# Kernel optimization log

Hardware: AMD Instinct MI355X
Metric: run time of the kernel (lower is better)

## Reference

```python
import jax, jax.numpy as jnp
import numpy as np

B, FEAT = 2048, 256
NUM_PIDS, CQ_SIZE = 30000, 8192
MOMENTUM = 0.5
SCALAR = 30.0
EPS_BN = 1e-5      # BatchNorm1d default eps
EPS_NORM = 1e-12   # F.normalize default eps


def l2norm(x):
    n = jnp.linalg.norm(x, axis=1, keepdims=True)
    return x / jnp.maximum(n, EPS_NORM)


def setup_inputs() -> dict:
    key = jax.random.key(0)
    k1, k2, k3, k4 = jax.random.split(key, 4)
    inputs = jax.random.normal(k1, (B, FEAT), jnp.float32)
    label = jax.random.randint(k2, (B,), 0, NUM_PIDS + 1)  # NUM_PIDS == ignore_index
    lut = jax.random.normal(k3, (NUM_PIDS, FEAT), jnp.float32)
    cq = jax.random.normal(k4, (CQ_SIZE, FEAT), jnp.float32)
    bn_weight = jnp.ones((FEAT,), jnp.float32)
    bn_bias = jnp.zeros((FEAT,), jnp.float32)
    return {"inputs": inputs, "label": label, "lut": lut, "cq": cq,
            "bn_weight": bn_weight, "bn_bias": bn_bias}


def reference(inputs, label, lut, cq, bn_weight, bn_bias):
    dtype = inputs.dtype
    rows = jnp.arange(B)

    # --- eval-mode BN on inputs (running stats at init: mean=0, var=1) ---
    norm_inputs = inputs / jnp.sqrt(jnp.asarray(1.0 + EPS_BN, dtype)) * bn_weight + bn_bias

    # --- bad-row masks (rows that are all zero) ---
    bad_lut_mask = jnp.all(lut == 0, axis=1)            # [P]
    good_lut = ~bad_lut_mask
    lc = jnp.minimum(label, NUM_PIDS - 1)
    bad_pos_mask = (label < NUM_PIDS) & bad_lut_mask[lc]  # label hits a bad lut row

    # --- train-mode masked BN over good lut rows (momentum=1.0 => running stats = batch stats) ---
    gm = good_lut[:, None].astype(dtype)
    n = jnp.sum(gm)
    mean = jnp.sum(lut * gm, axis=0) / n
    var = jnp.sum(((lut - mean) ** 2) * gm, axis=0) / n  # biased var for normalization
    lut_bn = jnp.where(good_lut[:, None],
                       (lut - mean) / jnp.sqrt(var + EPS_BN) * bn_weight + bn_bias,
                       lut)
    # running stats update happens under the hood (detached); unbiased var
    rm1 = jax.lax.stop_gradient(mean)
    rv1 = jax.lax.stop_gradient(var * n / (n - 1.0))

    qn = l2norm(norm_inputs)                              # [B, F]
    out_lab = qn @ l2norm(lut_bn).T                       # [B, P]
    out_lab = jnp.where(bad_lut_mask[None, :], jnp.asarray(-1.0, dtype), out_lab)
    out_lab = out_lab.at[rows, lc].set(
        jnp.where(bad_pos_mask, jnp.asarray(1.0, dtype), out_lab[rows, lc]))

    # --- eval-mode masked BN on cq using the just-updated running stats ---
    bad_cq_mask = jnp.all(cq == 0, axis=1)                # [Q]
    cq_bn = jnp.where(~bad_cq_mask[:, None],
                      (cq - rm1) / jnp.sqrt(rv1 + EPS_BN) * bn_weight + bn_bias,
                      cq)
    out_unl = qn @ l2norm(cq_bn).T                        # [B, Q]
    out_unl = jnp.where(bad_cq_mask[None, :], jnp.asarray(-1.0, dtype), out_unl)

    projected = jnp.concatenate([out_lab, out_unl], axis=1) * jnp.asarray(SCALAR, dtype)

    # --- cross entropy with ignore_index = NUM_PIDS, reduction='none', then sum/B ---
    logp = jax.nn.log_softmax(projected, axis=1)
    valid = label != NUM_PIDS
    per = -logp[rows, jnp.where(valid, label, 0)]
    per = jnp.where(valid, per, jnp.asarray(0.0, dtype))
    loss = jnp.sum(per) / B

    # --- serial momentum scatter into lut + circular-buffer enqueue into cq ---
    xs = jax.lax.stop_gradient(inputs)
    lut0 = jax.lax.stop_gradient(lut)
    cq0 = jax.lax.stop_gradient(cq)

    def step(carry, xy):
        lut_c, cq_c, hdr = carry
        x, y = xy
        is_lab = y < NUM_PIDS
        yc = jnp.minimum(y, NUM_PIDS - 1)
        new_row = jnp.where(is_lab, MOMENTUM * lut_c[yc] + (1.0 - MOMENTUM) * x, lut_c[yc])
        lut_c = lut_c.at[yc].set(new_row)
        cq_row = jnp.where(is_lab, cq_c[hdr], x)
        cq_c = cq_c.at[hdr].set(cq_row)
        hdr = jnp.where(is_lab, hdr, (hdr + 1) % CQ_SIZE)
        return (lut_c, cq_c, hdr), None

    (new_lut, new_cq, _), _ = jax.lax.scan(
        step, (lut0, cq0, jnp.asarray(0, label.dtype)), (xs, label))

    return loss, new_lut, new_cq
```

## Files before the change

### kernel.cpp

```cpp
#include <hip/hip_runtime.h>
#include <math.h>

#define NUM_PIDS 30000
#define CQ_SIZE  8192
#define BATCH    2048
#define FEAT     256
#define EPS_BN   1e-5f
#define EPS_NORM 1e-12f
#define SCALARV  30.0f

#define LUT_PAD  30080
#define NCOL     38272
#define BC       128
#define LUT_TILES 235
#define CT       299
#define RT       16
#define NWG      (CT*RT)
#define NB1      240
#define ROWS1    125
#define QPLANE   (BATCH*FEAT)

#define WS_Q1    0
#define WS_CB1   (WS_Q1 + BATCH*FEAT)
#define WS_CB2   (WS_CB1 + BATCH)
#define WS_RN2   (WS_CB2 + BATCH)
#define WS_FLAGS (WS_RN2 + 2*NCOL)
#define WS_PSUM  (WS_FLAGS + LUT_PAD)
#define WS_PSQ   (WS_PSUM + NB1*FEAT)
#define WS_PCNT  (WS_PSQ + NB1*FEAT)
#define WS_A1    (WS_PCNT + 256)
#define WS_B1    (WS_A1 + FEAT)
#define WS_A2    (WS_B1 + FEAT)
#define WS_B2    (WS_A2 + FEAT)
#define WS_ZT    (WS_B2 + FEAT)
#define WS_PART  (WS_ZT + BATCH)
#define WS_LOSS8 (WS_PART + BATCH*CT)
#define WS_XH    ((WS_LOSS8 + 8 + 3) & ~3)
#define WS_XL    (WS_XH + NCOL*FEAT/2)
#define WS_QP    (WS_XL + NCOL*FEAT/2)

typedef __bf16 bf16x8 __attribute__((ext_vector_type(8)));
typedef float  f32x4  __attribute__((ext_vector_type(4)));

__device__ __forceinline__ unsigned short f2bf(float f) {
  __bf16 h = (__bf16)f; return __builtin_bit_cast(unsigned short, h);
}
__device__ __forceinline__ float bf2f(unsigned short u) {
  __bf16 h = __builtin_bit_cast(__bf16, u); return (float)h;
}
__device__ __forceinline__ void gload_lds16(const void* g, void* l) {
  __builtin_amdgcn_global_load_lds((__attribute__((address_space(1))) void*)(g),
                                   (__attribute__((address_space(3))) void*)(l), 16, 0, 0);
}
__device__ __forceinline__ void stage8(const unsigned short* g, unsigned char* d) {
#pragma unroll
  for (int i = 0; i < 8; ++i)
    gload_lds16(g + (size_t)i * 16 * FEAT, d + i * 1024);
}

__global__ __launch_bounds__(256) void k_stats1(const float* __restrict__ lut,
                                                float* __restrict__ ws,
                                                int* __restrict__ flags) {
  const int t = threadIdx.x;
  const int rbase = blockIdx.x * ROWS1;
  __shared__ unsigned char wz[ROWS1 * 4];
  float s = 0.f, sq = 0.f;
  for (int i = 0; i < ROWS1; ++i) {
    float v = lut[(size_t)(rbase + i) * FEAT + t];
    s += v; sq += v * v;
    unsigned long long bal = __ballot(v != 0.0f);
    if ((t & 63) == 0) wz[i * 4 + (t >> 6)] = (bal != 0ull) ? 1 : 0;
  }
  __syncthreads();
  for (int i = t; i < ROWS1; i += 256) {
    int bad = !(wz[i*4] | wz[i*4+1] | wz[i*4+2] | wz[i*4+3]);
    flags[rbase + i] = bad;
  }
  ws[WS_PSUM + blockIdx.x * FEAT + t] = s;
  ws[WS_PSQ  + blockIdx.x * FEAT + t] = sq;
  if (t == 0) {
    int cnt = 0;
    for (int i = 0; i < ROWS1; ++i)
      cnt += (wz[i*4] | wz[i*4+1] | wz[i*4+2] | wz[i*4+3]) ? 1 : 0;
    ws[WS_PCNT + blockIdx.x] = (float)cnt;
  }
}

__global__ __launch_bounds__(256) void k_stats2(const float* __restrict__ bnw,
                                                const float* __restrict__ bnb,
                                                float* __restrict__ ws) {
  const int t = threadIdx.x;
  float2* rn2 = (float2*)(ws + WS_RN2);
  float s = 0.f, sq = 0.f, n = 0.f;
  for (int b = 0; b < NB1; ++b) { s += ws[WS_PSUM + b*FEAT + t]; sq += ws[WS_PSQ + b*FEAT + t]; }
  for (int b = 0; b < NB1; ++b) n += ws[WS_PCNT + b];
  float mean = s / n;
  float var = fmaxf(sq / n - mean * mean, 0.f);
  float istd_b = rsqrtf(var + EPS_BN);
  float rv1 = var * n / (n - 1.f);
  float istd_u = rsqrtf(rv1 + EPS_BN);
  float w = bnw[t], b_ = bnb[t];
  float a1 = istd_b * w, a2 = istd_u * w;
  ws[WS_A1 + t] = a1; ws[WS_B1 + t] = b_ - mean * a1;
  ws[WS_A2 + t] = a2; ws[WS_B2 + t] = b_ - mean * a2;
  if (t < (LUT_PAD - NUM_PIDS)) rn2[NUM_PIDS + t] = make_float2(0.f, -1e30f);
}

__global__ __launch_bounds__(256) void k_split(const float* __restrict__ lut,
                                               const float* __restrict__ cq,
                                               unsigned short* __restrict__ xh,
                                               unsigned short* __restrict__ xl) {
  const int stride = gridDim.x * blockDim.x;
  for (int u = blockIdx.x * blockDim.x + threadIdx.x; u < NCOL * 32; u += stride) {
    int col = u >> 5, k8 = (u & 31) * 8;
    float v[8];
    if (col < NUM_PIDS) {
      const float4* p = (const float4*)&lut[(size_t)col * FEAT + k8];
      float4 a = p[0], b = p[1];
      v[0]=a.x; v[1]=a.y; v[2]=a.z; v[3]=a.w; v[4]=b.x; v[5]=b.y; v[6]=b.z; v[7]=b.w;
    } else if (col < LUT_PAD) {
#pragma unroll
      for (int j = 0; j < 8; ++j) v[j] = 0.f;
    } else {
      const float4* p = (const float4*)&cq[(size_t)(col - LUT_PAD) * FEAT + k8];
      float4 a = p[0], b = p[1];
      v[0]=a.x; v[1]=a.y; v[2]=a.z; v[3]=a.w; v[4]=b.x; v[5]=b.y; v[6]=b.z; v[7]=b.w;
    }
    unsigned int hp[4], lp[4];
#pragma unroll
    for (int j = 0; j < 4; ++j) {
      unsigned short h0 = f2bf(v[2*j]),   h1 = f2bf(v[2*j+1]);
      unsigned short l0 = f2bf(v[2*j]   - bf2f(h0));
      unsigned short l1 = f2bf(v[2*j+1] - bf2f(h1));
      hp[j] = (unsigned int)h0 | ((unsigned int)h1 << 16);
      lp[j] = (unsigned int)l0 | ((unsigned int)l1 << 16);
    }
    size_t off = (size_t)col * FEAT + k8;
    *(uint4*)(xh + off) = make_uint4(hp[0], hp[1], hp[2], hp[3]);
    *(uint4*)(xl + off) = make_uint4(lp[0], lp[1], lp[2], lp[3]);
  }
}

__global__ __launch_bounds__(256) void k_qn(const float* __restrict__ inp,
                                            const float* __restrict__ bnw,
                                            const float* __restrict__ bnb,
                                            float* __restrict__ ws,
                                            unsigned short* __restrict__ qp) {
  const int r = blockIdx.x, t = threadIdx.x;
  const float s0 = rsqrtf(1.0f + EPS_BN);
  float v = inp[(size_t)r * FEAT + t];
  float bn = v * (bnw[t] * s0) + bnb[t];
  float x = bn * bn;
  for (int o = 32; o; o >>= 1) x += __shfl_down(x, o);
  __shared__ float w4[4];
  __shared__ float w8[8];
  if ((t & 63) == 0) w4[t >> 6] = x;
  __syncthreads();
  float nsq = w4[0] + w4[1] + w4[2] + w4[3];
  float rinv = 1.0f / fmaxf(sqrtf(nsq), EPS_NORM);
  float qn = bn * rinv;
  float y1 = qn * ws[WS_B1 + t], y2 = qn * ws[WS_B2 + t];
  for (int o = 32; o; o >>= 1) { y1 += __shfl_down(y1, o); y2 += __shfl_down(y2, o); }
  if ((t & 63) == 0) { w8[t >> 6] = y1; w8[4 + (t >> 6)] = y2; }
  float q1 = qn * ws[WS_A1 + t], q2 = qn * ws[WS_A2 + t];
  ws[WS_Q1 + (size_t)r * FEAT + t] = q1;
  size_t o1 = (size_t)r * FEAT + t;
  unsigned short h1 = f2bf(q1), h2 = f2bf(q2);
  qp[0*QPLANE + o1] = h1;
  qp[1*QPLANE + o1] = f2bf(q1 - bf2f(h1));
  qp[2*QPLANE + o1] = h2;
  qp[3*QPLANE + o1] = f2bf(q2 - bf2f(h2));
  __syncthreads();
  if (t == 0) {
    ws[WS_CB1 + r] = w8[0] + w8[1] + w8[2] + w8[3];
    ws[WS_CB2 + r] = w8[4] + w8[5] + w8[6] + w8[7];
  }
}

__global__ __launch_bounds__(256) void k_norms(const float* __restrict__ lut,
                                               const float* __restrict__ cq,
                                               float* __restrict__ ws) {
  const int row = blockIdx.x * 4 + (threadIdx.x >> 6);
  const int ln = threadIdx.x & 63;
  if (row >= NUM_PIDS + CQ_SIZE) return;
  float2* rn2 = (float2*)(ws + WS_RN2);
  const float* src; const float* av; const float* bv; int cidx;
  if (row < NUM_PIDS) {
    src = lut + (size_t)row * FEAT; av = ws + WS_A1; bv = ws + WS_B1; cidx = row;
  } else {
    int q = row - NUM_PIDS;
    src = cq + (size_t)q * FEAT; av = ws + WS_A2; bv = ws + WS_B2; cidx = LUT_PAD + q;
  }
  float4 x = ((const float4*)src)[ln];
  float4 a = ((const float4*)av)[ln];
  float4 b = ((const float4*)bv)[ln];
  bool nz = (x.x != 0.f) || (x.y != 0.f) || (x.z != 0.f) || (x.w != 0.f);
  unsigned long long bal = __ballot(nz);
  float t0 = a.x*x.x + b.x, t1 = a.y*x.y + b.y, t2 = a.z*x.z + b.z, t3 = a.w*x.w + b.w;
  float ssum = t0*t0 + t1*t1 + t2*t2 + t3*t3;
  for (int o = 32; o; o >>= 1) ssum += __shfl_xor(ssum, o);
  if (ln == 0) {
    rn2[cidx] = (bal == 0ull) ? make_float2(0.f, -SCALARV)
                              : make_float2(1.0f / fmaxf(sqrtf(ssum), EPS_NORM), 1e30f);
  }
}

__global__ __launch_bounds__(256) void k_gemm(const unsigned short* __restrict__ xh,
                                              const unsigned short* __restrict__ xl,
                                              const unsigned short* __restrict__ qp,
                                              float* __restrict__ ws) {
  __shared__ __align__(16) unsigned char smem[65536];
  const int tid = threadIdx.x;
  const int w = tid >> 6, l = tid & 63;
  const int bid = blockIdx.x;
  const int sid = (bid & 7) * (NWG / 8) + (bid >> 3);
  const int colT = sid >> 4, rowT = sid & 15;
  const bool islut = colT < LUT_TILES;
  const int colbase = colT * BC;
  const int rowbase = rowT * 128;

  const unsigned short* qh = qp + (islut ? 0 : 2) * QPLANE;
  const unsigned short* ql = qh + QPLANE;

  const unsigned short* gsrc;
  unsigned char* lbase;
  int gbase;
  if (w == 0)      { gsrc = xh; lbase = smem;         gbase = colbase; }
  else if (w == 1) { gsrc = xl; lbase = smem + 16384; gbase = colbase; }
  else if (w == 2) { gsrc = qh; lbase = smem + 32768; gbase = rowbase; }
  else             { gsrc = ql; lbase = smem + 49152; gbase = rowbase; }

  const int kchunk = (l & 3) ^ ((l >> 4) & 3);
  const unsigned short* gp = gsrc + (size_t)(gbase + (l >> 2)) * FEAT + kchunk * 8;

  const int lc = l & 15, lk = l >> 4;
  const int wr = w >> 1, wc = w & 1;
  const int roff = (lk ^ ((lc >> 2) & 3)) * 16;

  f32x4 acc[4][4];
#pragma unroll
  for (int rf = 0; rf < 4; ++rf)
#pragma unroll
    for (int cf = 0; cf < 4; ++cf) { f32x4 z = {0.f,0.f,0.f,0.f}; acc[rf][cf] = z; }

  stage8(gp, lbase);
  for (int s = 0; s < 8; ++s) {
    const int cur = s & 1;
    if (s < 7) {
      stage8(gp + (s + 1) * 32, lbase + (cur ^ 1) * 8192);
      asm volatile("s_waitcnt vmcnt(8)" ::: "memory");
    } else {
      asm volatile("s_waitcnt vmcnt(0)" ::: "memory");
    }
    __builtin_amdgcn_s_barrier();
    __builtin_amdgcn_sched_barrier(0);
    bf16x8 ah[4], al[4], bh[4], bl[4];
#pragma unroll
    for (int rf = 0; rf < 4; ++rf) {
      int off = cur * 8192 + (wr * 64 + rf * 16 + lc) * 64 + roff;
      ah[rf] = *(const bf16x8*)(smem + 32768 + off);
      al[rf] = *(const bf16x8*)(smem + 49152 + off);
    }
#pragma unroll
    for (int cf = 0; cf < 4; ++cf) {
      int off = cur * 8192 + (wc * 64 + cf * 16 + lc) * 64 + roff;
      bh[cf] = *(const bf16x8*)(smem + off);
      bl[cf] = *(const bf16x8*)(smem + 16384 + off);
    }
#pragma unroll
    for (int rf = 0; rf < 4; ++rf)
#pragma unroll
      for (int cf = 0; cf < 4; ++cf) {
        acc[rf][cf] = __builtin_amdgcn_mfma_f32_16x16x32_bf16(ah[rf], bh[cf], acc[rf][cf], 0, 0, 0);
        acc[rf][cf] = __builtin_amdgcn_mfma_f32_16x16x32_bf16(ah[rf], bl[cf], acc[rf][cf], 0, 0, 0);
        acc[rf][cf] = __builtin_amdgcn_mfma_f32_16x16x32_bf16(al[rf], bh[cf], acc[rf][cf], 0, 0, 0);
      }
    if (s < 7) __builtin_amdgcn_s_barrier();
  }

  const float* cb = ws + (islut ? WS_CB1 : WS_CB2);
  const float2* rn2 = (const float2*)(ws + WS_RN2);
  float* red = (float*)smem;
#pragma unroll
  for (int rf = 0; rf < 4; ++rf) {
    float cbv[4];
#pragma unroll
    for (int r4 = 0; r4 < 4; ++r4)
      cbv[r4] = cb[rowbase + wr * 64 + rf * 16 + lk * 4 + r4];
    float part[4] = {0.f, 0.f, 0.f, 0.f};
#pragma unroll
    for (int cf = 0; cf < 4; ++cf) {
      float2 rc = rn2[colbase + wc * 64 + cf * 16 + lc];
#pragma unroll
      for (int r4 = 0; r4 < 4; ++r4) {
        float z = SCALARV * rc.x * (acc[rf][cf][r4] + cbv[r4]);
        z = fminf(z, rc.y);
        part[r4] += __expf(z - SCALARV);
      }
    }
#pragma unroll
    for (int r4 = 0; r4 < 4; ++r4) {
#pragma unroll
      for (int o = 1; o < 16; o <<= 1) part[r4] += __shfl_xor(part[r4], o);
      if (lc == 0) red[(wr * 64 + rf * 16 + lk * 4 + r4) * 2 + wc] = part[r4];
    }
  }
  __syncthreads();
  if (tid < 128) {
    float val = red[tid * 2] + red[tid * 2 + 1];
    ws[WS_PART + (size_t)colT * BATCH + rowbase + tid] = val;
  }
}

__global__ __launch_bounds__(256) void k_target(const int* __restrict__ label,
                                                const float* __restrict__ lut,
                                                float* __restrict__ ws) {
  const int r = blockIdx.x, t = threadIdx.x;
  const int* flags = (const int*)(ws + WS_FLAGS);
  const float2* rn2 = (const float2*)(ws + WS_RN2);
  int y = label[r];
  if (y >= NUM_PIDS) { if (t == 0) ws[WS_ZT + r] = 0.f; return; }
  if (flags[y] == 1) { if (t == 0) ws[WS_ZT + r] = SCALARV; return; }
  float x = ws[WS_Q1 + (size_t)r * FEAT + t] * lut[(size_t)y * FEAT + t];
  for (int o = 32; o; o >>= 1) x += __shfl_down(x, o);
  __shared__ float w4[4];
  if ((t & 63) == 0) w4[t >> 6] = x;
  __syncthreads();
  if (t == 0) {
    float dot = w4[0] + w4[1] + w4[2] + w4[3];
    ws[WS_ZT + r] = SCALARV * rn2[y].x * (dot + ws[WS_CB1 + r]);
  }
}

__global__ __launch_bounds__(256) void k_loss(const int* __restrict__ label,
                                              float* __restrict__ ws) {
  const int t = threadIdx.x;
  const int r = blockIdx.x * 256 + t;
  const int* flags = (const int*)(ws + WS_FLAGS);
  float ls = 0.f;
  int y = label[r];
  if (y < NUM_PIDS) {
    float ss = 0.f;
    const float* p = ws + WS_PART;
    for (int c = 0; c < CT; ++c) ss += p[(size_t)c * BATCH + r];
    if (flags[y] == 1) ss += 1.0f - __expf(-2.0f * SCALARV);
    ls = (SCALARV + __logf(ss)) - ws[WS_ZT + r];
  }
  for (int o = 32; o; o >>= 1) ls += __shfl_down(ls, o);
  __shared__ float w4[4];
  if ((t & 63) == 0) w4[t >> 6] = ls;
  __syncthreads();
  if (t == 0) ws[WS_LOSS8 + blockIdx.x] = w4[0] + w4[1] + w4[2] + w4[3];
}

__global__ void k_loss2(float* __restrict__ ws, float* __restrict__ out) {
  if (threadIdx.x == 0) {
    float s = 0.f;
    for (int i = 0; i < 8; ++i) s += ws[WS_LOSS8 + i];
    out[0] = s / (float)BATCH;
  }
}

__global__ __launch_bounds__(256) void k_lutupd(const int* __restrict__ label,
                                                const float* __restrict__ inp,
                                                const float* __restrict__ lut,
                                                float* __restrict__ out_lut) {
  const int r = blockIdx.x, t = threadIdx.x;
  const int y = label[r];
  if (y >= NUM_PIDS) return;
  __shared__ unsigned long long mask[32];
  const int wv = t >> 6, ln = t & 63;
#pragma unroll
  for (int it = 0; it < 8; ++it) {
    int i = it * 256 + wv * 64 + ln;
    unsigned long long bal = __ballot(label[i] == y);
    if (ln == 0) mask[it * 4 + wv] = bal;
  }
  __syncthreads();
  const int wr_ = r >> 6, br_ = r & 63;
  unsigned long long selfbit = 1ull << br_;
  bool after = (mask[wr_] & ~((selfbit - 1) | selfbit)) != 0ull;
  for (int w2 = wr_ + 1; w2 < 32; ++w2) after = after || (mask[w2] != 0ull);
  if (after) return;
  float f = lut[(size_t)y * FEAT + t];
  for (int w2 = 0; w2 <= wr_; ++w2) {
    unsigned long long m = mask[w2];
    if (w2 == wr_) m &= (selfbit - 1) | selfbit;
    while (m) {
      int b = __ffsll((unsigned long long)m) - 1;
      m &= m - 1;
      int rr = w2 * 64 + b;
      f = 0.5f * f + 0.5f * inp[(size_t)rr * FEAT + t];
    }
  }
  out_lut[(size_t)y * FEAT + t] = f;
}

__global__ __launch_bounds__(256) void k_cqupd(const int* __restrict__ label,
                                               const float* __restrict__ inp,
                                               float* __restrict__ out_cq) {
  const int r = blockIdx.x, t = threadIdx.x;
  if (label[r] != NUM_PIDS) return;
  __shared__ unsigned long long mask[32];
  const int wv = t >> 6, ln = t & 63;
#pragma unroll
  for (int it = 0; it < 8; ++it) {
    int i = it * 256 + wv * 64 + ln;
    unsigned long long bal = __ballot(label[i] == NUM_PIDS);
    if (ln == 0) mask[it * 4 + wv] = bal;
  }
  __syncthreads();
  const int wr_ = r >> 6, br_ = r & 63;
  int rank = 0;
  for (int w2 = 0; w2 < wr_; ++w2) rank += __popcll(mask[w2]);
  rank += __popcll(mask[wr_] & ((1ull << br_) - 1ull));
  out_cq[(size_t)rank * FEAT + t] = inp[(size_t)r * FEAT + t];
}

extern "C" void kernel_launch(void* const* d_in, const int* in_sizes, int n_in,
                              void* d_out, int out_size, void* d_ws, size_t ws_size,
                              hipStream_t stream) {
  const float* inp = (const float*)d_in[0];
  const int* label = (const int*)d_in[1];
  const float* lut = (const float*)d_in[2];
  const float* cq  = (const float*)d_in[3];
  const float* bnw = (const float*)d_in[4];
  const float* bnb = (const float*)d_in[5];
  float* out = (float*)d_out;
  float* ws  = (float*)d_ws;
  int* flags = (int*)(ws + WS_FLAGS);
  unsigned short* xh = (unsigned short*)(ws + WS_XH);
  unsigned short* xl = (unsigned short*)(ws + WS_XL);
  unsigned short* qp = (unsigned short*)(ws + WS_QP);

  float* out_lut = out + 1;
  float* out_cq  = out + 1 + (size_t)NUM_PIDS * FEAT;

  hipMemcpyAsync(out_lut, lut, (size_t)NUM_PIDS * FEAT * sizeof(float),
                 hipMemcpyDeviceToDevice, stream);
  hipMemcpyAsync(out_cq, cq, (size_t)CQ_SIZE * FEAT * sizeof(float),
                 hipMemcpyDeviceToDevice, stream);

  k_split<<<2048, 256, 0, stream>>>(lut, cq, xh, xl);
  k_stats1<<<NB1, 256, 0, stream>>>(lut, ws, flags);
  k_stats2<<<1, 256, 0, stream>>>(bnw, bnb, ws);
  k_qn<<<BATCH, 256, 0, stream>>>(inp, bnw, bnb, ws, qp);
  k_norms<<<(NUM_PIDS + CQ_SIZE + 3) / 4, 256, 0, stream>>>(lut, cq, ws);
  k_gemm<<<NWG, 256, 0, stream>>>(xh, xl, qp, ws);
  k_target<<<BATCH, 256, 0, stream>>>(label, lut, ws);
  k_loss<<<8, 256, 0, stream>>>(label, ws);
  k_loss2<<<1, 64, 0, stream>>>(ws, out);
  k_lutupd<<<BATCH, 256, 0, stream>>>(label, inp, lut, out_lut);
  k_cqupd<<<BATCH, 256, 0, stream>>>(label, inp, out_cq);
}
```

Measured before the change: 374.0 us.

## Fuse split and norm kernels; restructure GEMM to stage only B tiles in LDS

Merges the bf16 hi/lo split kernel and the row-norm kernel into one per-row prep kernel, so lut and cq are read once instead of twice and a launch is dropped. The GEMM now stages only the lut/cq hi/lo tiles in LDS, loading 64-wide K chunks with an XOR swizzle. The query operand is read directly from global memory into registers. LDS use is halved and launch bounds request 3 blocks per CU for more occupancy, but the double-buffered prefetch is gone, so loads and MFMA no longer overlap, and direct global query loads may add latency.

```diff
diff --git a/kernel.cpp b/kernel.cpp
--- a/kernel.cpp
+++ b/kernel.cpp
@@ -52,11 +52,6 @@
   __builtin_amdgcn_global_load_lds((__attribute__((address_space(1))) void*)(g),
                                    (__attribute__((address_space(3))) void*)(l), 16, 0, 0);
 }
-__device__ __forceinline__ void stage8(const unsigned short* g, unsigned char* d) {
-#pragma unroll
-  for (int i = 0; i < 8; ++i)
-    gload_lds16(g + (size_t)i * 16 * FEAT, d + i * 1024);
-}
 
 __global__ __launch_bounds__(256) void k_stats1(const float* __restrict__ lut,
                                                 float* __restrict__ ws,
@@ -106,38 +101,44 @@
   if (t < (LUT_PAD - NUM_PIDS)) rn2[NUM_PIDS + t] = make_float2(0.f, -1e30f);
 }
 
-__global__ __launch_bounds__(256) void k_split(const float* __restrict__ lut,
-                                               const float* __restrict__ cq,
-                                               unsigned short* __restrict__ xh,
-                                               unsigned short* __restrict__ xl) {
-  const int stride = gridDim.x * blockDim.x;
-  for (int u = blockIdx.x * blockDim.x + threadIdx.x; u < NCOL * 32; u += stride) {
-    int col = u >> 5, k8 = (u & 31) * 8;
-    float v[8];
-    if (col < NUM_PIDS) {
-      const float4* p = (const float4*)&lut[(size_t)col * FEAT + k8];
-      float4 a = p[0], b = p[1];
-      v[0]=a.x; v[1]=a.y; v[2]=a.z; v[3]=a.w; v[4]=b.x; v[5]=b.y; v[6]=b.z; v[7]=b.w;
-    } else if (col < LUT_PAD) {
-#pragma unroll
-      for (int j = 0; j < 8; ++j) v[j] = 0.f;
-    } else {
-      const float4* p = (const float4*)&cq[(size_t)(col - LUT_PAD) * FEAT + k8];
-      float4 a = p[0], b = p[1];
-      v[0]=a.x; v[1]=a.y; v[2]=a.z; v[3]=a.w; v[4]=b.x; v[5]=b.y; v[6]=b.z; v[7]=b.w;
-    }
-    unsigned int hp[4], lp[4];
-#pragma unroll
-    for (int j = 0; j < 4; ++j) {
-      unsigned short h0 = f2bf(v[2*j]),   h1 = f2bf(v[2*j+1]);
-      unsigned short l0 = f2bf(v[2*j]   - bf2f(h0));
-      unsigned short l1 = f2bf(v[2*j+1] - bf2f(h1));
-      hp[j] = (unsigned int)h0 | ((unsigned int)h1 << 16);
-      lp[j] = (unsigned int)l0 | ((unsigned int)l1 << 16);
-    }
-    size_t off = (size_t)col * FEAT + k8;
-    *(uint4*)(xh + off) = make_uint4(hp[0], hp[1], hp[2], hp[3]);
-    *(uint4*)(xl + off) = make_uint4(lp[0], lp[1], lp[2], lp[3]);
+__global__ __launch_bounds__(256) void k_prep(const float* __restrict__ lut,
+                                              const float* __restrict__ cq,
+                                              float* __restrict__ ws,
+                                              unsigned short* __restrict__ xh,
+                                              unsigned short* __restrict__ xl) {
+  const int row = blockIdx.x * 4 + (threadIdx.x >> 6);
+  const int ln = threadIdx.x & 63;
+  float2* rn2 = (float2*)(ws + WS_RN2);
+  if (row >= NUM_PIDS && row < LUT_PAD) {
+    uint2 z = make_uint2(0u, 0u);
+    *(uint2*)(xh + (size_t)row * FEAT + ln * 4) = z;
+    *(uint2*)(xl + (size_t)row * FEAT + ln * 4) = z;
+    return;
+  }
+  const float* src; const float* av; const float* bv;
+  if (row < NUM_PIDS) {
+    src = lut + (size_t)row * FEAT; av = ws + WS_A1; bv = ws + WS_B1;
+  } else {
+    src = cq + (size_t)(row - LUT_PAD) * FEAT; av = ws + WS_A2; bv = ws + WS_B2;
+  }
+  float4 x = ((const float4*)src)[ln];
+  float4 a = ((const float4*)av)[ln];
+  float4 b = ((const float4*)bv)[ln];
+  unsigned short h0 = f2bf(x.x), h1 = f2bf(x.y), h2 = f2bf(x.z), h3 = f2bf(x.w);
+  unsigned short l0 = f2bf(x.x - bf2f(h0)), l1 = f2bf(x.y - bf2f(h1));
+  unsigned short l2 = f2bf(x.z - bf2f(h2)), l3 = f2bf(x.w - bf2f(h3));
+  *(uint2*)(xh + (size_t)row * FEAT + ln * 4) =
+      make_uint2((unsigned)h0 | ((unsigned)h1 << 16), (unsigned)h2 | ((unsigned)h3 << 16));
+  *(uint2*)(xl + (size_t)row * FEAT + ln * 4) =
+      make_uint2((unsigned)l0 | ((unsigned)l1 << 16), (unsigned)l2 | ((unsigned)l3 << 16));
+  bool nz = (x.x != 0.f) || (x.y != 0.f) || (x.z != 0.f) || (x.w != 0.f);
+  unsigned long long bal = __ballot(nz);
+  float t0 = a.x*x.x + b.x, t1 = a.y*x.y + b.y, t2 = a.z*x.z + b.z, t3 = a.w*x.w + b.w;
+  float ssum = t0*t0 + t1*t1 + t2*t2 + t3*t3;
+  for (int o = 32; o; o >>= 1) ssum += __shfl_xor(ssum, o);
+  if (ln == 0) {
+    rn2[row] = (bal == 0ull) ? make_float2(0.f, -SCALARV)
+                             : make_float2(1.0f / fmaxf(sqrtf(ssum), EPS_NORM), 1e30f);
   }
 }
 
@@ -177,39 +178,11 @@
   }
 }
 
-__global__ __launch_bounds__(256) void k_norms(const float* __restrict__ lut,
-                                               const float* __restrict__ cq,
-                                               float* __restrict__ ws) {
-  const int row = blockIdx.x * 4 + (threadIdx.x >> 6);
-  const int ln = threadIdx.x & 63;
-  if (row >= NUM_PIDS + CQ_SIZE) return;
-  float2* rn2 = (float2*)(ws + WS_RN2);
-  const float* src; const float* av; const float* bv; int cidx;
-  if (row < NUM_PIDS) {
-    src = lut + (size_t)row * FEAT; av = ws + WS_A1; bv = ws + WS_B1; cidx = row;
-  } else {
-    int q = row - NUM_PIDS;
-    src = cq + (size_t)q * FEAT; av = ws + WS_A2; bv = ws + WS_B2; cidx = LUT_PAD + q;
-  }
-  float4 x = ((const float4*)src)[ln];
-  float4 a = ((const float4*)av)[ln];
-  float4 b = ((const float4*)bv)[ln];
-  bool nz = (x.x != 0.f) || (x.y != 0.f) || (x.z != 0.f) || (x.w != 0.f);
-  unsigned long long bal = __ballot(nz);
-  float t0 = a.x*x.x + b.x, t1 = a.y*x.y + b.y, t2 = a.z*x.z + b.z, t3 = a.w*x.w + b.w;
-  float ssum = t0*t0 + t1*t1 + t2*t2 + t3*t3;
-  for (int o = 32; o; o >>= 1) ssum += __shfl_xor(ssum, o);
-  if (ln == 0) {
-    rn2[cidx] = (bal == 0ull) ? make_float2(0.f, -SCALARV)
-                              : make_float2(1.0f / fmaxf(sqrtf(ssum), EPS_NORM), 1e30f);
-  }
-}
-
-__global__ __launch_bounds__(256) void k_gemm(const unsigned short* __restrict__ xh,
-                                              const unsigned short* __restrict__ xl,
-                                              const unsigned short* __restrict__ qp,
-                                              float* __restrict__ ws) {
-  __shared__ __align__(16) unsigned char smem[65536];
+__global__ __launch_bounds__(256, 3) void k_gemm(const unsigned short* __restrict__ xh,
+                                                 const unsigned short* __restrict__ xl,
+                                                 const unsigned short* __restrict__ qp,
+                                                 float* __restrict__ ws) {
+  __shared__ __align__(16) unsigned char smem[32768];
   const int tid = threadIdx.x;
   const int w = tid >> 6, l = tid & 63;
   const int bid = blockIdx.x;
@@ -222,20 +195,16 @@
   const unsigned short* qh = qp + (islut ? 0 : 2) * QPLANE;
   const unsigned short* ql = qh + QPLANE;
 
-  const unsigned short* gsrc;
-  unsigned char* lbase;
-  int gbase;
-  if (w == 0)      { gsrc = xh; lbase = smem;         gbase = colbase; }
-  else if (w == 1) { gsrc = xl; lbase = smem + 16384; gbase = colbase; }
-  else if (w == 2) { gsrc = qh; lbase = smem + 32768; gbase = rowbase; }
-  else             { gsrc = ql; lbase = smem + 49152; gbase = rowbase; }
-
-  const int kchunk = (l & 3) ^ ((l >> 4) & 3);
-  const unsigned short* gp = gsrc + (size_t)(gbase + (l >> 2)) * FEAT + kchunk * 8;
+  const unsigned short* sg = (w & 1) ? xl : xh;
+  unsigned char* sl = smem + (w & 1) * 16384 + (w >> 1) * 8192;
+  const int segc = l >> 3;
+  const int kc8l = (l & 7) ^ segc;
+  const unsigned short* gp =
+      sg + (size_t)(colbase + (w >> 1) * 64 + segc) * FEAT + kc8l * 8;
 
   const int lc = l & 15, lk = l >> 4;
   const int wr = w >> 1, wc = w & 1;
-  const int roff = (lk ^ ((lc >> 2) & 3)) * 16;
+  const size_t qbase = (size_t)(rowbase + wr * 64 + lc) * FEAT;
 
   f32x4 acc[4][4];
 #pragma unroll
@@ -243,39 +212,39 @@
 #pragma unroll
     for (int cf = 0; cf < 4; ++cf) { f32x4 z = {0.f,0.f,0.f,0.f}; acc[rf][cf] = z; }
 
-  stage8(gp, lbase);
-  for (int s = 0; s < 8; ++s) {
-    const int cur = s & 1;
-    if (s < 7) {
-      stage8(gp + (s + 1) * 32, lbase + (cur ^ 1) * 8192);
-      asm volatile("s_waitcnt vmcnt(8)" ::: "memory");
-    } else {
-      asm volatile("s_waitcnt vmcnt(0)" ::: "memory");
+  for (int kc = 0; kc < 4; ++kc) {
+    const int kb = kc * 64;
+#pragma unroll
+    for (int i = 0; i < 8; ++i)
+      gload_lds16(gp + (size_t)i * 8 * FEAT + kb, sl + i * 1024);
+    __syncthreads();
+#pragma unroll
+    for (int ks = 0; ks < 2; ++ks) {
+      const int kc8 = ks * 4 + lk;
+      const int sA = (kc8 ^ (lc & 7)) * 16;
+      bf16x8 ah[4], al[4], bh[4], bl[4];
+#pragma unroll
+      for (int rf = 0; rf < 4; ++rf) {
+        size_t qa = qbase + rf * 16 * FEAT + kb + kc8 * 8;
+        ah[rf] = *(const bf16x8*)(qh + qa);
+        al[rf] = *(const bf16x8*)(ql + qa);
+      }
+#pragma unroll
+      for (int cf = 0; cf < 4; ++cf) {
+        int off = (wc * 64 + cf * 16 + lc) * 128 + sA;
+        bh[cf] = *(const bf16x8*)(smem + off);
+        bl[cf] = *(const bf16x8*)(smem + 16384 + off);
+      }
+#pragma unroll
+      for (int rf = 0; rf < 4; ++rf)
+#pragma unroll
+        for (int cf = 0; cf < 4; ++cf) {
+          acc[rf][cf] = __builtin_amdgcn_mfma_f32_16x16x32_bf16(ah[rf], bh[cf], acc[rf][cf], 0, 0, 0);
+          acc[rf][cf] = __builtin_amdgcn_mfma_f32_16x16x32_bf16(ah[rf], bl[cf], acc[rf][cf], 0, 0, 0);
+          acc[rf][cf] = __builtin_amdgcn_mfma_f32_16x16x32_bf16(al[rf], bh[cf], acc[rf][cf], 0, 0, 0);
+        }
     }
-    __builtin_amdgcn_s_barrier();
-    __builtin_amdgcn_sched_barrier(0);
-    bf16x8 ah[4], al[4], bh[4], bl[4];
-#pragma unroll
-    for (int rf = 0; rf < 4; ++rf) {
-      int off = cur * 8192 + (wr * 64 + rf * 16 + lc) * 64 + roff;
-      ah[rf] = *(const bf16x8*)(smem + 32768 + off);
-      al[rf] = *(const bf16x8*)(smem + 49152 + off);
-    }
-#pragma unroll
-    for (int cf = 0; cf < 4; ++cf) {
-      int off = cur * 8192 + (wc * 64 + cf * 16 + lc) * 64 + roff;
-      bh[cf] = *(const bf16x8*)(smem + off);
-      bl[cf] = *(const bf16x8*)(smem + 16384 + off);
-    }
-#pragma unroll
-    for (int rf = 0; rf < 4; ++rf)
-#pragma unroll
-      for (int cf = 0; cf < 4; ++cf) {
-        acc[rf][cf] = __builtin_amdgcn_mfma_f32_16x16x32_bf16(ah[rf], bh[cf], acc[rf][cf], 0, 0, 0);
-        acc[rf][cf] = __builtin_amdgcn_mfma_f32_16x16x32_bf16(ah[rf], bl[cf], acc[rf][cf], 0, 0, 0);
-        acc[rf][cf] = __builtin_amdgcn_mfma_f32_16x16x32_bf16(al[rf], bh[cf], acc[rf][cf], 0, 0, 0);
-      }
-    if (s < 7) __builtin_amdgcn_s_barrier();
+    __syncthreads();
   }
 
   const float* cb = ws + (islut ? WS_CB1 : WS_CB2);
@@ -441,11 +410,10 @@
   hipMemcpyAsync(out_cq, cq, (size_t)CQ_SIZE * FEAT * sizeof(float),
                  hipMemcpyDeviceToDevice, stream);
 
-  k_split<<<2048, 256, 0, stream>>>(lut, cq, xh, xl);
   k_stats1<<<NB1, 256, 0, stream>>>(lut, ws, flags);
   k_stats2<<<1, 256, 0, stream>>>(bnw, bnb, ws);
+  k_prep<<<NCOL / 4, 256, 0, stream>>>(lut, cq, ws, xh, xl);
   k_qn<<<BATCH, 256, 0, stream>>>(inp, bnw, bnb, ws, qp);
-  k_norms<<<(NUM_PIDS + CQ_SIZE + 3) / 4, 256, 0, stream>>>(lut, cq, ws);
   k_gemm<<<NWG, 256, 0, stream>>>(xh, xl, qp, ws);
   k_target<<<BATCH, 256, 0, stream>>>(label, lut, ws);
   k_loss<<<8, 256, 0, stream>>>(label, ws);
```

Result: slower. 383.3 us (+2.5%).
